# Optimization experiments

Measured on AMD Instinct MI355X. Metric: run time of the kernel, lower is better.

## Reference

```python
import jax, jax.numpy as jnp
import numpy as np

B, S, D, H = 8, 1024, 1024, 16
DH = D // H


def setup_inputs() -> dict:
    key = jax.random.key(0)
    ks = jax.random.split(key, 8)
    en = jax.random.normal(ks[0], (B, S, D), dtype=jnp.float32)
    fr = jax.random.normal(ks[1], (B, S, D), dtype=jnp.float32)
    l_en = jax.random.randint(ks[2], (B,), 1, S + 1)
    l_fr = jax.random.randint(ks[3], (B,), 1, S + 1)
    # nn.Linear-style params (weight stored [out, in])
    lim_q = 1.0 / np.sqrt(D)
    W_Q_w = jax.random.uniform(ks[4], (D, D), minval=-lim_q, maxval=lim_q, dtype=jnp.float32)
    W_Q_b = jax.random.uniform(ks[5], (D,), minval=-lim_q, maxval=lim_q, dtype=jnp.float32)
    W_KV_w = jax.random.uniform(ks[6], (2 * D, D), minval=-lim_q, maxval=lim_q, dtype=jnp.float32)
    W_KV_b = jax.random.uniform(ks[7], (2 * D,), minval=-lim_q, maxval=lim_q, dtype=jnp.float32)
    return {"en": en, "fr": fr, "l_en": l_en, "l_fr": l_fr,
            "W_Q_w": W_Q_w, "W_Q_b": W_Q_b, "W_KV_w": W_KV_w, "W_KV_b": W_KV_b}


def reference(en, fr, l_en, l_fr, W_Q_w, W_Q_b, W_KV_w, W_KV_b):
    # q from decoder (fr), k/v from encoder (en)
    q = (fr @ W_Q_w.T + W_Q_b).reshape(B, S, H, DH).transpose(0, 2, 1, 3)  # [B,H,S,DH]
    kv = (en @ W_KV_w.T + W_KV_b).reshape(B, S, 2, H, DH).transpose(2, 0, 3, 1, 4)
    k, v = kv[0], kv[1]  # [B,H,S,DH]

    # NOTE: original scales by sqrt(embedding_dim), not sqrt(head_dim)
    attn = jnp.einsum('bhqd,bhkd->bhqk', q, k) / jnp.sqrt(jnp.float32(D))

    pos = jnp.arange(S)
    mask_en = (pos[None, :] < l_en[:, None])  # [B,S] key mask
    mask_fr = (pos[None, :] < l_fr[:, None])  # [B,S] query mask
    mask = (mask_fr[:, :, None] & mask_en[:, None, :])[:, None, :, :]  # [B,1,Sq,Sk]

    attn = jnp.where(mask, attn, -jnp.inf)
    attn = jax.nn.softmax(attn, axis=-1)
    attn = jnp.nan_to_num(attn)  # fully-masked rows -> 0 (matches torch nan_to_num)

    out = jnp.einsum('bhqk,bhkd->bhqd', attn, v)  # [B,H,S,DH]
    return out.transpose(0, 2, 1, 3).reshape(B, S, D)
```

## Files before the change

kernel.cpp:

```cpp
#include <hip/hip_runtime.h>
#include <hip/hip_bf16.h>
#include <stdint.h>

typedef __bf16 bf16_t;
typedef bf16_t bf16x8 __attribute__((ext_vector_type(8)));
typedef float f32x4 __attribute__((ext_vector_type(4)));
typedef unsigned short ushortx8 __attribute__((ext_vector_type(8)));

__device__ __forceinline__ uint16_t f2bf(float f) {
  uint32_t u = __float_as_uint(f);
  uint32_t r = u + 0x7FFFu + ((u >> 16) & 1u);
  return (uint16_t)(r >> 16);
}

__device__ __forceinline__ int read_len(const int* __restrict__ p, int b) {
  bool is64 = (p[1] == 0) | (p[3] == 0) | (p[5] == 0) | (p[7] == 0);
  return is64 ? p[2 * b] : p[b];
}

#define GLDS16(gp, lp)                                                   \
  __builtin_amdgcn_global_load_lds(                                      \
      (const __attribute__((address_space(1))) uint32_t*)(gp),           \
      (__attribute__((address_space(3))) uint32_t*)(lp), 16, 0, 0)

__global__ void cvt4_kernel(const float* __restrict__ s0, uint16_t* __restrict__ d0, int n0,
                            const float* __restrict__ s1, uint16_t* __restrict__ d1, int n1,
                            const float* __restrict__ s2, uint16_t* __restrict__ d2, int n2,
                            const float* __restrict__ s3, uint16_t* __restrict__ d3, int n3,
                            const int* __restrict__ msk2, const int* __restrict__ msk3) {
  int e = (blockIdx.x * blockDim.x + threadIdx.x) * 4;
  const float* s;
  uint16_t* d;
  const int* msk = nullptr;
  if (e < n0) { s = s0 + e; d = d0 + e; }
  else if ((e -= n0) < n1) { s = s1 + e; d = d1 + e; }
  else if ((e -= n1) < n2) { s = s2 + e; d = d2 + e; msk = msk2; }
  else if ((e -= n2) < n3) { s = s3 + e; d = d3 + e; msk = msk3; }
  else return;
  if (msk) {
    int row = (e >> 10) & 1023, b = e >> 20;
    int need = (read_len(msk, b) + 127) & ~127;
    if (row >= need) return;
  }
  const float4 v = *reinterpret_cast<const float4*>(s);
  ushort4 o;
  o.x = f2bf(v.x); o.y = f2bf(v.y); o.z = f2bf(v.z); o.w = f2bf(v.w);
  *reinterpret_cast<ushort4*>(d) = o;
}

template <bool ABF16>
__global__ __launch_bounds__(256) void gemm_fused(
    const float* __restrict__ frF, const float* __restrict__ enF,
    const uint16_t* __restrict__ frB, const uint16_t* __restrict__ enB,
    const uint16_t* __restrict__ wq, const uint16_t* __restrict__ wkv,
    const float* __restrict__ bq, const float* __restrict__ bkv,
    const int* __restrict__ l_en_p, const int* __restrict__ l_fr_p,
    uint16_t* __restrict__ Qb,
    uint16_t* __restrict__ Kb,
    uint16_t* __restrict__ Vb) {
  __shared__ __attribute__((aligned(16))) uint16_t As[2][128 * 64];
  __shared__ __attribute__((aligned(16))) uint16_t Bs[2][128 * 64];
  const int t = threadIdx.x;
  const int lane = t & 63;
  const int w = t >> 6;
  const int wm = w >> 1, wn = w & 1;
  const int l15 = lane & 15, lg = lane >> 4;

  const int orig = blockIdx.x;
  const int xcd = orig & 7;
  const int slot = orig >> 3;
  const bool isQ = slot < 64;
  int b, bn;
  if (isQ) { b = slot >> 3; bn = (slot & 7) * 128; }
  else { int s2 = slot - 64; b = s2 >> 4; bn = (s2 & 15) * 128; }
  const int i = (xcd - b) & 7;
  const int bm = b * 1024 + i * 128;

  const int need = isQ ? read_len(l_fr_p, b) : read_len(l_en_p, b);
  if (i * 128 >= need) return;

  const uint16_t* Bw = isQ ? wq : wkv;
  const float* bias = isQ ? bq : bkv;
  const float scale = isQ ? 0.03125f : 1.0f;
  const uint16_t* Ab = isQ ? frB : enB;
  const float* Af = isQ ? frF : enF;

  f32x4 acc[4][4];
#pragma unroll
  for (int ii = 0; ii < 4; ++ii)
#pragma unroll
    for (int j = 0; j < 4; ++j) acc[ii][j] = (f32x4){0.f, 0.f, 0.f, 0.f};

  float4 ar0[4], ar1[4];

  auto stageB = [&](int buf, int kt) {
#pragma unroll
    for (int ii = 0; ii < 4; ++ii) {
      int g = t + 256 * ii;
      int L = g ^ ((g >> 3) & 7);
      int row = L >> 3, k8 = L & 7;
      GLDS16(Bw + (size_t)(bn + row) * 1024 + kt + k8 * 8, &Bs[buf][g * 8]);
    }
  };
  auto stageA_bf = [&](int buf, int kt) {
#pragma unroll
    for (int ii = 0; ii < 4; ++ii) {
      int g = t + 256 * ii;
      int L = g ^ ((g >> 3) & 7);
      int row = L >> 3, k8 = L & 7;
      GLDS16(Ab + (size_t)(bm + row) * 1024 + kt + k8 * 8, &As[buf][g * 8]);
    }
  };
  auto loadA_f32 = [&](int kt) {
#pragma unroll
    for (int ii = 0; ii < 4; ++ii) {
      int L = t + 256 * ii;
      int row = L >> 3, k8 = L & 7;
      const float* src = Af + (size_t)(bm + row) * 1024 + kt + k8 * 8;
      ar0[ii] = *reinterpret_cast<const float4*>(src);
      ar1[ii] = *reinterpret_cast<const float4*>(src + 4);
    }
  };
  auto writeA = [&](int buf) {
#pragma unroll
    for (int ii = 0; ii < 4; ++ii) {
      int L = t + 256 * ii;
      int row = L >> 3, k8 = L & 7;
      ushortx8 o;
      o[0] = f2bf(ar0[ii].x); o[1] = f2bf(ar0[ii].y);
      o[2] = f2bf(ar0[ii].z); o[3] = f2bf(ar0[ii].w);
      o[4] = f2bf(ar1[ii].x); o[5] = f2bf(ar1[ii].y);
      o[6] = f2bf(ar1[ii].z); o[7] = f2bf(ar1[ii].w);
      int byte = (row * 128 + k8 * 16) ^ ((row & 7) << 4);
      *reinterpret_cast<ushortx8*>(reinterpret_cast<char*>(As[buf]) + byte) = o;
    }
  };
  auto compute = [&](int buf) {
#pragma unroll
    for (int ks = 0; ks < 2; ++ks) {
      const int kb = ks * 64 + lg * 16;
      bf16x8 af[4], bf[4];
#pragma unroll
      for (int mf = 0; mf < 4; ++mf) {
        int row = wm * 64 + mf * 16 + l15;
        int byte = (row * 128 + kb) ^ ((row & 7) << 4);
        af[mf] = *reinterpret_cast<const bf16x8*>(
            reinterpret_cast<const char*>(As[buf]) + byte);
      }
#pragma unroll
      for (int nf = 0; nf < 4; ++nf) {
        int row = wn * 64 + nf * 16 + l15;
        int byte = (row * 128 + kb) ^ ((row & 7) << 4);
        bf[nf] = *reinterpret_cast<const bf16x8*>(
            reinterpret_cast<const char*>(Bs[buf]) + byte);
      }
#pragma unroll
      for (int mf = 0; mf < 4; ++mf)
#pragma unroll
        for (int nf = 0; nf < 4; ++nf)
          acc[mf][nf] = __builtin_amdgcn_mfma_f32_16x16x32_bf16(
              af[mf], bf[nf], acc[mf][nf], 0, 0, 0);
    }
  };

  if (ABF16) {
    stageB(0, 0);
    stageA_bf(0, 0);
  } else {
    loadA_f32(0);
    stageB(0, 0);
    writeA(0);
  }
  __syncthreads();

#pragma unroll 2
  for (int tt = 0; tt < 16; ++tt) {
    const int cur = tt & 1;
    const int ktn = (tt + 1) * 64;
    if (ABF16) {
      if (tt < 15) { stageB(cur ^ 1, ktn); stageA_bf(cur ^ 1, ktn); }
      compute(cur);
    } else {
      if (tt < 15) { stageB(cur ^ 1, ktn); loadA_f32(ktn); }
      compute(cur);
      if (tt < 15) writeA(cur ^ 1);
    }
    __syncthreads();
  }

#pragma unroll
  for (int mf = 0; mf < 4; ++mf) {
#pragma unroll
    for (int nf = 0; nf < 4; ++nf) {
      int n = bn + wn * 64 + nf * 16 + l15;
      float bv = bias[n];
#pragma unroll
      for (int r = 0; r < 4; ++r) {
        int m = bm + wm * 64 + mf * 16 + lg * 4 + r;
        float v = (acc[mf][nf][r] + bv) * scale;
        uint16_t o = f2bf(v);
        int bb = m >> 10, s = m & 1023;
        if (isQ) {
          int h = n >> 6, d = n & 63;
          Qb[((((bb * 16 + h) << 10) | s) << 6) | d] = o;
        } else if (n < 1024) {
          int h = n >> 6, d = n & 63;
          Kb[((((bb * 16 + h) << 10) | s) << 6) | d] = o;
        } else {
          int n2 = n - 1024;
          int h = n2 >> 6, d = n2 & 63;
          Vb[((((bb * 16 + h) << 6) | d) << 10) | s] = o;
        }
      }
    }
  }
}

__global__ __launch_bounds__(512) void attn_kernel(
    const uint16_t* __restrict__ Qb,
    const uint16_t* __restrict__ Kb,
    const uint16_t* __restrict__ Vt,
    const int* __restrict__ l_en_p, const int* __restrict__ l_fr_p,
    float* __restrict__ out) {
  __shared__ __attribute__((aligned(16))) uint16_t Ks[2][64 * 64];
  __shared__ __attribute__((aligned(16))) uint16_t Vs[2][64 * 64];
  __shared__ __attribute__((aligned(16))) bf16_t Ps[8][16][72];
  const int t = threadIdx.x;
  const int lane = t & 63, w = t >> 6;
  const int l15 = lane & 15, lg = lane >> 4;
  const int orig = blockIdx.x;
  const int xcd = orig & 7;
  const int slot = orig >> 3;
  const int b = slot >> 4;
  const int rest = slot & 15;
  const int h = xcd + 8 * (rest >> 3);
  const int q0 = (rest & 7) << 7;
  const int bh = b * 16 + h;
  const int len_en = read_len(l_en_p, b);
  const int len_fr = read_len(l_fr_p, b);

  if (q0 >= len_fr) {
    for (int i = t; i < 128 * 64; i += 512) {
      int rr = i >> 6, cc = i & 63;
      out[(size_t)(b * 1024 + q0 + rr) * 1024 + h * 64 + cc] = 0.f;
    }
    return;
  }

  const uint16_t* qbase =
      Qb + ((size_t)bh * 1024 + q0 + w * 16 + l15) * 64 + lg * 8;
  const bf16x8 aq0 = *reinterpret_cast<const bf16x8*>(qbase);
  const bf16x8 aq1 = *reinterpret_cast<const bf16x8*>(qbase + 32);

  float mrow[4], lrow[4];
  f32x4 oacc[4];
#pragma unroll
  for (int r = 0; r < 4; ++r) { mrow[r] = -1e30f; lrow[r] = 0.f; }
#pragma unroll
  for (int df = 0; df < 4; ++df) oacc[df] = (f32x4){0.f, 0.f, 0.f, 0.f};

  auto stage = [&](int buf, int j0) {
    int g = t;
    int L = g ^ ((g >> 3) & 7);
    int row = L >> 3, k8 = L & 7;
    GLDS16(Kb + ((size_t)bh * 1024 + j0 + row) * 64 + k8 * 8, &Ks[buf][g * 8]);
    GLDS16(Vt + ((size_t)bh * 64 + row) * 1024 + j0 + k8 * 8, &Vs[buf][g * 8]);
  };

  const int ntiles = (len_en + 63) >> 6;
  stage(0, 0);
  __syncthreads();

  for (int tt = 0; tt < ntiles; ++tt) {
    const int cur = tt & 1;
    const int j0 = tt * 64;
    if (tt + 1 < ntiles) stage(cur ^ 1, (tt + 1) * 64);

    f32x4 sc[4];
#pragma unroll
    for (int nf = 0; nf < 4; ++nf) sc[nf] = (f32x4){0.f, 0.f, 0.f, 0.f};
#pragma unroll
    for (int ks = 0; ks < 2; ++ks) {
      const bf16x8 aq = ks ? aq1 : aq0;
      const int kb = ks * 64 + lg * 16;
#pragma unroll
      for (int nf = 0; nf < 4; ++nf) {
        int row = nf * 16 + l15;
        int byte = (row * 128 + kb) ^ ((row & 7) << 4);
        bf16x8 bk = *reinterpret_cast<const bf16x8*>(
            reinterpret_cast<const char*>(Ks[cur]) + byte);
        sc[nf] = __builtin_amdgcn_mfma_f32_16x16x32_bf16(aq, bk, sc[nf], 0, 0, 0);
      }
    }
#pragma unroll
    for (int nf = 0; nf < 4; ++nf) {
      int col = j0 + nf * 16 + l15;
      if (col >= len_en) sc[nf] = (f32x4){-1e30f, -1e30f, -1e30f, -1e30f};
    }
    float tm[4];
#pragma unroll
    for (int r = 0; r < 4; ++r)
      tm[r] = fmaxf(fmaxf(sc[0][r], sc[1][r]), fmaxf(sc[2][r], sc[3][r]));
#pragma unroll
    for (int off = 1; off < 16; off <<= 1)
#pragma unroll
      for (int r = 0; r < 4; ++r) tm[r] = fmaxf(tm[r], __shfl_xor(tm[r], off));

    bool small = (tm[0] <= mrow[0] + 8.f) && (tm[1] <= mrow[1] + 8.f) &&
                 (tm[2] <= mrow[2] + 8.f) && (tm[3] <= mrow[3] + 8.f);
    if (!__all(small)) {
      float fac[4];
#pragma unroll
      for (int r = 0; r < 4; ++r) {
        float mn = fmaxf(mrow[r], tm[r]);
        fac[r] = __expf(mrow[r] - mn);
        mrow[r] = mn;
      }
#pragma unroll
      for (int r = 0; r < 4; ++r) lrow[r] *= fac[r];
#pragma unroll
      for (int df = 0; df < 4; ++df)
#pragma unroll
        for (int r = 0; r < 4; ++r) oacc[df][r] *= fac[r];
    }
    float ps[4] = {0.f, 0.f, 0.f, 0.f};
#pragma unroll
    for (int nf = 0; nf < 4; ++nf)
#pragma unroll
      for (int r = 0; r < 4; ++r) {
        float p = __expf(sc[nf][r] - mrow[r]);
        ps[r] += p;
        Ps[w][lg * 4 + r][nf * 16 + l15] = (bf16_t)p;
      }
#pragma unroll
    for (int off = 1; off < 16; off <<= 1)
#pragma unroll
      for (int r = 0; r < 4; ++r) ps[r] += __shfl_xor(ps[r], off);
#pragma unroll
    for (int r = 0; r < 4; ++r) lrow[r] += ps[r];

#pragma unroll
    for (int ks = 0; ks < 2; ++ks) {
      const bf16x8 pa = *reinterpret_cast<const bf16x8*>(
          &Ps[w][l15][0] + ks * 32 + lg * 8);
#pragma unroll
      for (int df = 0; df < 4; ++df) {
        int row = df * 16 + l15;
        int byte = (row * 128 + ks * 64 + lg * 16) ^ ((row & 7) << 4);
        bf16x8 bv = *reinterpret_cast<const bf16x8*>(
            reinterpret_cast<const char*>(Vs[cur]) + byte);
        oacc[df] = __builtin_amdgcn_mfma_f32_16x16x32_bf16(pa, bv, oacc[df], 0, 0, 0);
      }
    }
    __syncthreads();
  }

#pragma unroll
  for (int df = 0; df < 4; ++df)
#pragma unroll
    for (int r = 0; r < 4; ++r) {
      int q = q0 + w * 16 + lg * 4 + r;
      float inv = (q < len_fr && lrow[r] > 0.f) ? 1.0f / lrow[r] : 0.f;
      out[(size_t)(b * 1024 + q) * 1024 + h * 64 + df * 16 + l15] =
          oacc[df][r] * inv;
    }
}

extern "C" void kernel_launch(void* const* d_in, const int* in_sizes, int n_in,
                              void* d_out, int out_size, void* d_ws,
                              size_t ws_size, hipStream_t stream) {
  const float* en = (const float*)d_in[0];
  const float* fr = (const float*)d_in[1];
  const int* l_en = (const int*)d_in[2];
  const int* l_fr = (const int*)d_in[3];
  const float* wq = (const float*)d_in[4];
  const float* bq = (const float*)d_in[5];
  const float* wkv = (const float*)d_in[6];
  const float* bkv = (const float*)d_in[7];
  float* out = (float*)d_out;

  char* ws = (char*)d_ws;
  uint16_t* wq_bf = (uint16_t*)(ws);
  uint16_t* wkv_bf = (uint16_t*)(ws + 2097152);
  uint16_t* Qbuf = (uint16_t*)(ws + 6291456);
  uint16_t* Kbuf = (uint16_t*)(ws + 23068672);
  uint16_t* Vtbuf = (uint16_t*)(ws + 39845888);
  uint16_t* fr_bf = (uint16_t*)(ws + 56623104);
  uint16_t* en_bf = (uint16_t*)(ws + 73400320);
  const bool pre = ws_size >= 90177536ull;

  if (pre) {
    cvt4_kernel<<<19456, 256, 0, stream>>>(wq, wq_bf, 1048576,
                                           wkv, wkv_bf, 2097152,
                                           fr, fr_bf, 8388608,
                                           en, en_bf, 8388608,
                                           l_fr, l_en);
    gemm_fused<true><<<1536, 256, 0, stream>>>(nullptr, nullptr, fr_bf, en_bf,
                                               wq_bf, wkv_bf, bq, bkv,
                                               l_en, l_fr, Qbuf, Kbuf, Vtbuf);
  } else {
    cvt4_kernel<<<3072, 256, 0, stream>>>(wq, wq_bf, 1048576,
                                          wkv, wkv_bf, 2097152,
                                          nullptr, nullptr, 0,
                                          nullptr, nullptr, 0,
                                          nullptr, nullptr);
    gemm_fused<false><<<1536, 256, 0, stream>>>(fr, en, nullptr, nullptr,
                                                wq_bf, wkv_bf, bq, bkv,
                                                l_en, l_fr, Qbuf, Kbuf, Vtbuf);
  }

  attn_kernel<<<1024, 512, 0, stream>>>(Qbuf, Kbuf, Vtbuf, l_en, l_fr, out);
}
```

Baseline: 115.6 us.

## Triple-buffer weight tiles with vmcnt-based waits in GEMM; raise MFMA priority in attention

In the bf16-A GEMM path, the weight (B) tiles now use three LDS buffers and are prefetched two k-steps ahead, while A stays double-buffered. __syncthreads is replaced by explicit s_waitcnt vmcnt and s_barrier so outstanding loads for later tiles can stay in flight across the barrier. The attention kernel wraps its MFMA sections in s_setprio to favour matrix work among co-resident waves. The extra B buffer raises LDS use, which may lower occupancy, and the hand-written vmcnt counts have to match the number of loads issued per stage.

Result: no change. 115.5 us (-0.0%).

```diff
diff --git a/kernel.cpp b/kernel.cpp
--- a/kernel.cpp
+++ b/kernel.cpp
@@ -59,7 +59,7 @@
     uint16_t* __restrict__ Kb,
     uint16_t* __restrict__ Vb) {
   __shared__ __attribute__((aligned(16))) uint16_t As[2][128 * 64];
-  __shared__ __attribute__((aligned(16))) uint16_t Bs[2][128 * 64];
+  __shared__ __attribute__((aligned(16))) uint16_t Bs[ABF16 ? 3 : 2][128 * 64];
   const int t = threadIdx.x;
   const int lane = t & 63;
   const int w = t >> 6;
@@ -91,8 +91,6 @@
 #pragma unroll
     for (int j = 0; j < 4; ++j) acc[ii][j] = (f32x4){0.f, 0.f, 0.f, 0.f};
 
-  float4 ar0[4], ar1[4];
-
   auto stageB = [&](int buf, int kt) {
 #pragma unroll
     for (int ii = 0; ii < 4; ++ii) {
@@ -111,31 +109,7 @@
       GLDS16(Ab + (size_t)(bm + row) * 1024 + kt + k8 * 8, &As[buf][g * 8]);
     }
   };
-  auto loadA_f32 = [&](int kt) {
-#pragma unroll
-    for (int ii = 0; ii < 4; ++ii) {
-      int L = t + 256 * ii;
-      int row = L >> 3, k8 = L & 7;
-      const float* src = Af + (size_t)(bm + row) * 1024 + kt + k8 * 8;
-      ar0[ii] = *reinterpret_cast<const float4*>(src);
-      ar1[ii] = *reinterpret_cast<const float4*>(src + 4);
-    }
-  };
-  auto writeA = [&](int buf) {
-#pragma unroll
-    for (int ii = 0; ii < 4; ++ii) {
-      int L = t + 256 * ii;
-      int row = L >> 3, k8 = L & 7;
-      ushortx8 o;
-      o[0] = f2bf(ar0[ii].x); o[1] = f2bf(ar0[ii].y);
-      o[2] = f2bf(ar0[ii].z); o[3] = f2bf(ar0[ii].w);
-      o[4] = f2bf(ar1[ii].x); o[5] = f2bf(ar1[ii].y);
-      o[6] = f2bf(ar1[ii].z); o[7] = f2bf(ar1[ii].w);
-      int byte = (row * 128 + k8 * 16) ^ ((row & 7) << 4);
-      *reinterpret_cast<ushortx8*>(reinterpret_cast<char*>(As[buf]) + byte) = o;
-    }
-  };
-  auto compute = [&](int buf) {
+  auto computeAB = [&](int bufA, int bufB) {
 #pragma unroll
     for (int ks = 0; ks < 2; ++ks) {
       const int kb = ks * 64 + lg * 16;
@@ -145,14 +119,14 @@
         int row = wm * 64 + mf * 16 + l15;
         int byte = (row * 128 + kb) ^ ((row & 7) << 4);
         af[mf] = *reinterpret_cast<const bf16x8*>(
-            reinterpret_cast<const char*>(As[buf]) + byte);
+            reinterpret_cast<const char*>(As[bufA]) + byte);
       }
 #pragma unroll
       for (int nf = 0; nf < 4; ++nf) {
         int row = wn * 64 + nf * 16 + l15;
         int byte = (row * 128 + kb) ^ ((row & 7) << 4);
         bf[nf] = *reinterpret_cast<const bf16x8*>(
-            reinterpret_cast<const char*>(Bs[buf]) + byte);
+            reinterpret_cast<const char*>(Bs[bufB]) + byte);
       }
 #pragma unroll
       for (int mf = 0; mf < 4; ++mf)
@@ -164,28 +138,65 @@
   };
 
   if (ABF16) {
+    stageA_bf(0, 0);
     stageB(0, 0);
-    stageA_bf(0, 0);
+    stageB(1, 64);
+    asm volatile("s_waitcnt vmcnt(4)" ::: "memory");
+    __builtin_amdgcn_s_barrier();
+    __builtin_amdgcn_sched_barrier(0);
+    int bA = 0, bB = 0;
+    for (int tt = 0; tt < 16; ++tt) {
+      if (tt + 1 < 16) stageA_bf(bA ^ 1, (tt + 1) * 64);
+      if (tt + 2 < 16) stageB(bB >= 1 ? bB - 1 : bB + 2, (tt + 2) * 64);
+      computeAB(bA, bB);
+      if (tt < 15) {
+        if (tt < 14) asm volatile("s_waitcnt vmcnt(4)" ::: "memory");
+        else         asm volatile("s_waitcnt vmcnt(0)" ::: "memory");
+        __builtin_amdgcn_s_barrier();
+        __builtin_amdgcn_sched_barrier(0);
+      }
+      bA ^= 1;
+      bB = (bB == 2) ? 0 : bB + 1;
+    }
   } else {
+    float4 ar0[4], ar1[4];
+    auto loadA_f32 = [&](int kt) {
+#pragma unroll
+      for (int ii = 0; ii < 4; ++ii) {
+        int L = t + 256 * ii;
+        int row = L >> 3, k8 = L & 7;
+        const float* src = Af + (size_t)(bm + row) * 1024 + kt + k8 * 8;
+        ar0[ii] = *reinterpret_cast<const float4*>(src);
+        ar1[ii] = *reinterpret_cast<const float4*>(src + 4);
+      }
+    };
+    auto writeA = [&](int buf) {
+#pragma unroll
+      for (int ii = 0; ii < 4; ++ii) {
+        int L = t + 256 * ii;
+        int row = L >> 3, k8 = L & 7;
+        ushortx8 o;
+        o[0] = f2bf(ar0[ii].x); o[1] = f2bf(ar0[ii].y);
+        o[2] = f2bf(ar0[ii].z); o[3] = f2bf(ar0[ii].w);
+        o[4] = f2bf(ar1[ii].x); o[5] = f2bf(ar1[ii].y);
+        o[6] = f2bf(ar1[ii].z); o[7] = f2bf(ar1[ii].w);
+        int byte = (row * 128 + k8 * 16) ^ ((row & 7) << 4);
+        *reinterpret_cast<ushortx8*>(reinterpret_cast<char*>(As[buf]) + byte) = o;
+      }
+    };
     loadA_f32(0);
     stageB(0, 0);
     writeA(0);
-  }
-  __syncthreads();
-
+    __syncthreads();
 #pragma unroll 2
-  for (int tt = 0; tt < 16; ++tt) {
-    const int cur = tt & 1;
-    const int ktn = (tt + 1) * 64;
-    if (ABF16) {
-      if (tt < 15) { stageB(cur ^ 1, ktn); stageA_bf(cur ^ 1, ktn); }
-      compute(cur);
-    } else {
+    for (int tt = 0; tt < 16; ++tt) {
+      const int cur = tt & 1;
+      const int ktn = (tt + 1) * 64;
       if (tt < 15) { stageB(cur ^ 1, ktn); loadA_f32(ktn); }
-      compute(cur);
+      computeAB(cur, cur);
       if (tt < 15) writeA(cur ^ 1);
-    }
-    __syncthreads();
+      __syncthreads();
+    }
   }
 
 #pragma unroll
@@ -279,6 +290,7 @@
     f32x4 sc[4];
 #pragma unroll
     for (int nf = 0; nf < 4; ++nf) sc[nf] = (f32x4){0.f, 0.f, 0.f, 0.f};
+    __builtin_amdgcn_s_setprio(1);
 #pragma unroll
     for (int ks = 0; ks < 2; ++ks) {
       const bf16x8 aq = ks ? aq1 : aq0;
@@ -292,6 +304,7 @@
         sc[nf] = __builtin_amdgcn_mfma_f32_16x16x32_bf16(aq, bk, sc[nf], 0, 0, 0);
       }
     }
+    __builtin_amdgcn_s_setprio(0);
 #pragma unroll
     for (int nf = 0; nf < 4; ++nf) {
       int col = j0 + nf * 16 + l15;
@@ -339,6 +352,7 @@
 #pragma unroll
     for (int r = 0; r < 4; ++r) lrow[r] += ps[r];
 
+    __builtin_amdgcn_s_setprio(1);
 #pragma unroll
     for (int ks = 0; ks < 2; ++ks) {
       const bf16x8 pa = *reinterpret_cast<const bf16x8*>(
@@ -352,6 +366,7 @@
         oacc[df] = __builtin_amdgcn_mfma_f32_16x16x32_bf16(pa, bv, oacc[df], 0, 0, 0);
       }
     }
+    __builtin_amdgcn_s_setprio(0);
     __syncthreads();
   }
 
```
